# Performance work log

Measured on AMD Instinct MI355X. Metric: run time of the kernel, lower is better.

Reference implementation:

```python
import jax, jax.numpy as jnp
import numpy as np

# Faithful JAX port of approxmatch.cu / matchcost.cu (Fan et al., PointSetGeneration),
# as wrapped by emd_cuda_confidence in the torch module.

def _sqdist(xyz1, xyz2):
    # xyz1 (n,3), xyz2 (m,3) -> (n,m) squared euclidean distances
    return jnp.sum((xyz1[:, None, :] - xyz2[None, :, :]) ** 2, axis=-1)


def _approxmatch(xyz1, xyz2):
    # Iterative soft bipartite matching with annealed temperature levels
    # level = -4^j for j = 7..-1, then level = 0 (10 iterations total).
    n, m = xyz1.shape[0], xyz2.shape[0]
    sqd = _sqdist(xyz1, xyz2)  # (n, m)
    # CUDA: multiL = max(1, m/n) (int div), multiR = max(1, n/m)
    multiL = float(max(1, m // n))
    multiR = float(max(1, n // m))
    levels = jnp.asarray([-(4.0 ** j) for j in range(7, -2, -1)] + [0.0],
                         dtype=jnp.float32)
    match0 = jnp.zeros((n, m), jnp.float32)
    remL0 = jnp.full((n,), multiL, jnp.float32)
    remR0 = jnp.full((m,), multiR, jnp.float32)

    def step(carry, level):
        match, remL, remR = carry
        W = jnp.exp(level * sqd)                       # (n, m) affinity
        ratioL = remL / (1e-9 + W @ remR)              # (n,)
        ratioR = remR / (1e-9 + W.T @ ratioL)          # (m,)
        delta = W * ratioL[:, None] * ratioR[None, :]  # mass moved this level
        match = match + delta
        remL = jnp.maximum(0.0, remL - delta.sum(axis=1))
        remR = jnp.maximum(0.0, remR - delta.sum(axis=0))
        return (match, remL, remR), None

    (match, _, _), _ = jax.lax.scan(step, (match0, remL0, remR0), levels)
    return match  # (n, m)


def _matchcost(xyz1, xyz2, match):
    d = jnp.sqrt(_sqdist(xyz1, xyz2))  # euclidean distance, (n, m)
    return jnp.sum(match * d)


def setup_inputs() -> dict:
    key = jax.random.key(0)
    k1, k2 = jax.random.split(key)
    xyz1 = jax.random.normal(k1, (8, 2048, 3), dtype=jnp.float32)
    xyz2 = jax.random.normal(k2, (8, 2048, 3), dtype=jnp.float32)
    return {"xyz1": xyz1, "xyz2": xyz2}


def reference(xyz1, xyz2):
    match = jax.vmap(_approxmatch)(xyz1, xyz2)          # (b, n, m)
    cost = jax.vmap(_matchcost)(xyz1, xyz2, match)       # (b,)
    # CUDA kernel stores match with layout (b, m, n) (index k*n+l)
    return cost, jnp.swapaxes(match, 1, 2)
```

## Files before the change

### kernel.cpp

```cpp
#include <hip/hip_runtime.h>
#include <math.h>

#define B_ 8
#define N_ 2048
static constexpr int BN = B_ * N_;
static constexpr int THREADS = 256;
static constexpr int WPC = 64;
static constexpr int ROWS_PER_WG = N_ / WPC;
static constexpr int RG = 8;
static constexpr int NSTRIPE = THREADS / RG;
static constexpr int JPER = N_ / NSTRIPE;

#if __has_builtin(__builtin_amdgcn_exp2f)
#define FEXP2(x) __builtin_amdgcn_exp2f(x)
#else
#define FEXP2(x) exp2f(x)
#endif

template<int MODE>
__global__ __launch_bounds__(THREADS)
void pass_kernel(const float* __restrict__ xyz1, const float* __restrict__ xyz2,
                 float* __restrict__ ws, float* __restrict__ outCost,
                 float cA, float cB, int lvl)
{
    __shared__ float4 pts[N_];
    __shared__ float rem2[(MODE==2) ? N_ : 1];
    __shared__ float red1[4][RG][4];
    __shared__ float red2[4][RG][4];

    float* remL = ws;
    float* remR = ws + BN;
    float* ratL = ws + 2*BN;
    float* ratR = ws + 12*BN;

    const int wg = blockIdx.x;
    const int b = wg / WPC;
    const int wloc = wg - b*WPC;
    const int t = threadIdx.x;

    if (MODE==0 && wg==0 && t < B_) outCost[t] = 0.0f;

    const float* colxyz = (MODE==1) ? xyz1 : xyz2;
    const float* rowxyz = (MODE==1) ? xyz2 : xyz1;
    const float* wvec   = (MODE==1) ? (ratL + (size_t)lvl*BN)
                        : (MODE==2) ? (ratR + (size_t)lvl*BN) : nullptr;

    for (int j = t; j < N_; j += THREADS) {
        const float* p = colxyz + (size_t)(b*N_ + j)*3;
        float w = (MODE==0) ? 0.0f : wvec[b*N_ + j];
        pts[j] = make_float4(p[0], p[1], p[2], w);
        if (MODE==2) rem2[j] = remR[b*N_ + j];
    }

    const int rg = t & (RG-1);
    const int stripe = t >> 3;
    const int rowbase = wloc*ROWS_PER_WG + rg*4;
    float rx[4], ry[4], rz[4];
    #pragma unroll
    for (int r = 0; r < 4; ++r) {
        const float* q = rowxyz + (size_t)(b*N_ + rowbase + r)*3;
        rx[r] = q[0]; ry[r] = q[1]; rz[r] = q[2];
    }
    __syncthreads();

    float acc1[4] = {0.f,0.f,0.f,0.f};
    float acc2[4] = {0.f,0.f,0.f,0.f};
    const int jbase = stripe * JPER;
    const int jrot  = 2*stripe;
    for (int jj = 0; jj < JPER; ++jj) {
        const int j = jbase + ((jj + jrot) & (JPER-1));
        const float4 p = pts[j];
        float rr = 0.f;
        if (MODE==2) rr = rem2[j];
        #pragma unroll
        for (int r = 0; r < 4; ++r) {
            float dx = rx[r]-p.x, dy = ry[r]-p.y, dz = rz[r]-p.z;
            float sqd = fmaf(dx,dx, fmaf(dy,dy, dz*dz));
            float w1 = FEXP2(cA*sqd);
            if (MODE==0) acc1[r] += w1;
            else         acc1[r] = fmaf(w1, p.w, acc1[r]);
            if (MODE==2) {
                float w2 = FEXP2(cB*sqd);
                acc2[r] = fmaf(w2, rr, acc2[r]);
            }
        }
    }

    #pragma unroll
    for (int r = 0; r < 4; ++r) {
        float v = acc1[r];
        v += __shfl_xor(v, 8); v += __shfl_xor(v, 16); v += __shfl_xor(v, 32);
        acc1[r] = v;
        if (MODE==2) {
            float u = acc2[r];
            u += __shfl_xor(u, 8); u += __shfl_xor(u, 16); u += __shfl_xor(u, 32);
            acc2[r] = u;
        }
    }
    const int wave = t >> 6, lane = t & 63;
    if (lane < RG) {
        #pragma unroll
        for (int r = 0; r < 4; ++r) {
            red1[wave][lane][r] = acc1[r];
            if (MODE==2) red2[wave][lane][r] = acc2[r];
        }
    }
    __syncthreads();
    if (t < ROWS_PER_WG) {
        const int rgf = t >> 2, ri = t & 3;
        float s1 = red1[0][rgf][ri]+red1[1][rgf][ri]+red1[2][rgf][ri]+red1[3][rgf][ri];
        const int gi = b*N_ + wloc*ROWS_PER_WG + rgf*4 + ri;
        if (MODE==0) {
            ratL[gi] = 1.0f / (1e-9f + s1);
            remL[gi] = 1.0f;
            remR[gi] = 1.0f;
        } else if (MODE==1) {
            float rr  = remR[gi];
            float rat = rr / (1e-9f + s1);
            ratR[(size_t)lvl*BN + gi] = rat;
            remR[gi] = fmaxf(0.0f, rr - rat*s1);
        } else {
            float s2 = red2[0][rgf][ri]+red2[1][rgf][ri]+red2[2][rgf][ri]+red2[3][rgf][ri];
            float rl  = remL[gi];
            float rlo = ratL[(size_t)lvl*BN + gi];
            float nl  = fmaxf(0.0f, rl - rlo*s1);
            remL[gi] = nl;
            ratL[(size_t)(lvl+1)*BN + gi] = nl / (1e-9f + s2);
        }
    }
}

static constexpr int MT  = 256;
static constexpr int JCH = 256;

__global__ __launch_bounds__(MT)
void match_kernel(const float* __restrict__ xyz1, const float* __restrict__ xyz2,
                  const float* __restrict__ ws, float* __restrict__ out, float c0)
{
    __shared__ float4 pts[JCH];
    __shared__ float rr[10][JCH];
    __shared__ float cred[MT/64];

    const float* ratL = ws + 2*BN;
    const float* ratR = ws + 12*BN;
    float* outCost  = out;
    float* outMatch = out + B_;

    const int wg = blockIdx.x;
    const int b  = wg >> 6;
    const int jc = (wg >> 3) & 7;
    const int ic = wg & 7;
    const int t  = threadIdx.x;

    const int i = ic*MT + t;
    const float* q = xyz1 + (size_t)(b*N_ + i)*3;
    const float x1 = q[0], y1 = q[1], z1 = q[2];
    float RL[10];
    #pragma unroll
    for (int l = 0; l < 10; ++l) RL[l] = ratL[(size_t)l*BN + b*N_ + i];

    {
        const int gj = jc*JCH + t;
        const float* p = xyz2 + (size_t)(b*N_ + gj)*3;
        pts[t] = make_float4(p[0], p[1], p[2], 0.f);
        #pragma unroll
        for (int l = 0; l < 10; ++l) rr[l][t] = ratR[(size_t)l*BN + b*N_ + gj];
    }
    __syncthreads();

    float cost = 0.f;
    const size_t obase = (size_t)b*N_*N_ + (size_t)(jc*JCH)*N_ + (size_t)(ic*MT) + t;
    for (int jj = 0; jj < JCH; ++jj) {
        const float4 p = pts[jj];
        float dx = x1-p.x, dy = y1-p.y, dz = z1-p.z;
        float sqd = fmaf(dx,dx, fmaf(dy,dy, dz*dz));
        float m = 0.f;
        float arg = c0*sqd;
        #pragma unroll
        for (int l = 0; l < 9; ++l) {
            float w = FEXP2(arg);
            m = fmaf(w * RL[l], rr[l][jj], m);
            arg *= 0.25f;
        }
        m = fmaf(RL[9], rr[9][jj], m);
        outMatch[obase + (size_t)jj*N_] = m;
        cost = fmaf(m, sqrtf(sqd), cost);
    }

    #pragma unroll
    for (int s = 1; s < 64; s <<= 1) cost += __shfl_xor(cost, s);
    const int wave = t >> 6, lane = t & 63;
    if (lane == 0) cred[wave] = cost;
    __syncthreads();
    if (t == 0) {
        float v = cred[0]+cred[1]+cred[2]+cred[3];
        atomicAdd(outCost + b, v);
    }
}

extern "C" void kernel_launch(void* const* d_in, const int* in_sizes, int n_in,
                              void* d_out, int out_size, void* d_ws, size_t ws_size,
                              hipStream_t stream) {
    const float* xyz1 = (const float*)d_in[0];
    const float* xyz2 = (const float*)d_in[1];
    float* out = (float*)d_out;
    float* ws  = (float*)d_ws;

    const double L2E = 1.4426950408889634;
    float c[10];
    for (int l = 0; l < 9; ++l) c[l] = (float)(-pow(4.0, 7 - l) * L2E);
    c[9] = 0.0f;

    dim3 grid(B_*WPC), blk(THREADS);
    pass_kernel<0><<<grid, blk, 0, stream>>>(xyz1, xyz2, ws, out, c[0], 0.f, 0);
    for (int l = 0; l < 10; ++l) {
        pass_kernel<1><<<grid, blk, 0, stream>>>(xyz1, xyz2, ws, out, c[l], 0.f, l);
        if (l < 9)
            pass_kernel<2><<<grid, blk, 0, stream>>>(xyz1, xyz2, ws, out, c[l], c[l+1], l);
    }
    match_kernel<<<dim3(B_*64), dim3(MT), 0, stream>>>(xyz1, xyz2, ws, out, c[0]);
}
```

Baseline: 486.5 us.

## Skip underflowed exp terms, expand distances algebraically, specialize final levels, retile match

The pass kernel is rewritten so each wave handles four rows over all columns. Squared distances come from an expanded dot-product form, and wave-uniform checks skip exp evaluation when every exponent is below the float underflow threshold. The last level (c=0) is special-cased: its row sum becomes a plain sum of remR, and ratR for that level comes from a small closed-form reduction kernel instead of a full pass. The match kernel is retiled so each thread covers 4 rows over 32 columns, and it exits the level chain early once the weights underflow. It also uses nontemporal stores and derives sqrt distances from the scaled argument, which adds cancellation error from the expanded-distance form.

```diff
diff --git a/kernel.cpp b/kernel.cpp
--- a/kernel.cpp
+++ b/kernel.cpp
@@ -5,11 +5,8 @@
 #define N_ 2048
 static constexpr int BN = B_ * N_;
 static constexpr int THREADS = 256;
-static constexpr int WPC = 64;
+static constexpr int WPC = 128;
 static constexpr int ROWS_PER_WG = N_ / WPC;
-static constexpr int RG = 8;
-static constexpr int NSTRIPE = THREADS / RG;
-static constexpr int JPER = N_ / NSTRIPE;
 
 #if __has_builtin(__builtin_amdgcn_exp2f)
 #define FEXP2(x) __builtin_amdgcn_exp2f(x)
@@ -17,71 +14,79 @@
 #define FEXP2(x) exp2f(x)
 #endif
 
-template<int MODE>
-__global__ __launch_bounds__(THREADS)
+template<int MODE, bool CB0>
+__global__ __launch_bounds__(THREADS, 4)
 void pass_kernel(const float* __restrict__ xyz1, const float* __restrict__ xyz2,
                  float* __restrict__ ws, float* __restrict__ outCost,
-                 float cA, float cB, int lvl)
+                 float cA, float skipTh, int lvl)
 {
     __shared__ float4 pts[N_];
     __shared__ float rem2[(MODE==2) ? N_ : 1];
-    __shared__ float red1[4][RG][4];
-    __shared__ float red2[4][RG][4];
 
     float* remL = ws;
     float* remR = ws + BN;
     float* ratL = ws + 2*BN;
     float* ratR = ws + 12*BN;
 
-    const int wg = blockIdx.x;
-    const int b = wg / WPC;
-    const int wloc = wg - b*WPC;
-    const int t = threadIdx.x;
+    const int wg   = blockIdx.x;
+    const int b    = wg >> 7;
+    const int wloc = wg & 127;
+    const int t    = threadIdx.x;
 
     if (MODE==0 && wg==0 && t < B_) outCost[t] = 0.0f;
 
     const float* colxyz = (MODE==1) ? xyz1 : xyz2;
     const float* rowxyz = (MODE==1) ? xyz2 : xyz1;
     const float* wvec   = (MODE==1) ? (ratL + (size_t)lvl*BN)
-                        : (MODE==2) ? (ratR + (size_t)lvl*BN) : nullptr;
-
-    for (int j = t; j < N_; j += THREADS) {
+                        : (ratR + (size_t)lvl*BN);
+
+    #pragma unroll
+    for (int k = 0; k < N_/THREADS; ++k) {
+        const int j = t + k*THREADS;
         const float* p = colxyz + (size_t)(b*N_ + j)*3;
-        float w = (MODE==0) ? 0.0f : wvec[b*N_ + j];
+        float w = 0.0f;
+        if (MODE != 0) w = wvec[b*N_ + j];
         pts[j] = make_float4(p[0], p[1], p[2], w);
-        if (MODE==2) rem2[j] = remR[b*N_ + j];
-    }
-
-    const int rg = t & (RG-1);
-    const int stripe = t >> 3;
-    const int rowbase = wloc*ROWS_PER_WG + rg*4;
-    float rx[4], ry[4], rz[4];
+        if (MODE == 2) rem2[j] = remR[b*N_ + j];
+    }
+
+    const int wave = t >> 6, lane = t & 63;
+    const int rowbase = wloc*ROWS_PER_WG + wave*4;
+    float ax[4], ay[4], az[4], aq[4];
     #pragma unroll
     for (int r = 0; r < 4; ++r) {
         const float* q = rowxyz + (size_t)(b*N_ + rowbase + r)*3;
-        rx[r] = q[0]; ry[r] = q[1]; rz[r] = q[2];
+        const float qx = q[0], qy = q[1], qz = q[2];
+        ax[r] = -2.0f*cA*qx; ay[r] = -2.0f*cA*qy; az[r] = -2.0f*cA*qz;
+        aq[r] = cA * fmaf(qx,qx, fmaf(qy,qy, qz*qz));
     }
     __syncthreads();
 
     float acc1[4] = {0.f,0.f,0.f,0.f};
     float acc2[4] = {0.f,0.f,0.f,0.f};
-    const int jbase = stripe * JPER;
-    const int jrot  = 2*stripe;
-    for (int jj = 0; jj < JPER; ++jj) {
-        const int j = jbase + ((jj + jrot) & (JPER-1));
+    float sumRem = 0.f;
+
+    #pragma unroll 4
+    for (int jj = 0; jj < 32; ++jj) {
+        const int j = (lane << 5) | ((jj + lane) & 31);
         const float4 p = pts[j];
-        float rr = 0.f;
-        if (MODE==2) rr = rem2[j];
-        #pragma unroll
-        for (int r = 0; r < 4; ++r) {
-            float dx = rx[r]-p.x, dy = ry[r]-p.y, dz = rz[r]-p.z;
-            float sqd = fmaf(dx,dx, fmaf(dy,dy, dz*dz));
-            float w1 = FEXP2(cA*sqd);
-            if (MODE==0) acc1[r] += w1;
-            else         acc1[r] = fmaf(w1, p.w, acc1[r]);
-            if (MODE==2) {
-                float w2 = FEXP2(cB*sqd);
-                acc2[r] = fmaf(w2, rr, acc2[r]);
+        if (MODE==2 && CB0) sumRem += rem2[j];
+        const float cpp = cA * fmaf(p.x,p.x, fmaf(p.y,p.y, p.z*p.z));
+        float a[4];
+        #pragma unroll
+        for (int r = 0; r < 4; ++r)
+            a[r] = fmaf(ax[r],p.x, fmaf(ay[r],p.y, fmaf(az[r],p.z, cpp + aq[r])));
+        const float amax = fmaxf(fmaxf(a[0],a[1]), fmaxf(a[2],a[3]));
+        if (__any(amax >= skipTh)) {
+            float rr = 0.f;
+            if (MODE==2 && !CB0) rr = rem2[j];
+            #pragma unroll
+            for (int r = 0; r < 4; ++r) {
+                const float w1 = FEXP2(a[r]);
+                if (MODE==0) acc1[r] += w1;
+                else         acc1[r] = fmaf(w1, p.w, acc1[r]);
+                if (MODE==2 && !CB0)
+                    acc2[r] = fmaf(FEXP2(a[r]*0.25f), rr, acc2[r]);
             }
         }
     }
@@ -89,57 +94,75 @@
     #pragma unroll
     for (int r = 0; r < 4; ++r) {
         float v = acc1[r];
-        v += __shfl_xor(v, 8); v += __shfl_xor(v, 16); v += __shfl_xor(v, 32);
+        #pragma unroll
+        for (int s = 1; s < 64; s <<= 1) v += __shfl_xor(v, s);
         acc1[r] = v;
-        if (MODE==2) {
+        if (MODE==2 && !CB0) {
             float u = acc2[r];
-            u += __shfl_xor(u, 8); u += __shfl_xor(u, 16); u += __shfl_xor(u, 32);
+            #pragma unroll
+            for (int s = 1; s < 64; s <<= 1) u += __shfl_xor(u, s);
             acc2[r] = u;
         }
     }
-    const int wave = t >> 6, lane = t & 63;
-    if (lane < RG) {
+    if (MODE==2 && CB0) {
+        float u = sumRem;
+        #pragma unroll
+        for (int s = 1; s < 64; s <<= 1) u += __shfl_xor(u, s);
+        sumRem = u;
+    }
+
+    if (lane == 0) {
         #pragma unroll
         for (int r = 0; r < 4; ++r) {
-            red1[wave][lane][r] = acc1[r];
-            if (MODE==2) red2[wave][lane][r] = acc2[r];
-        }
-    }
-    __syncthreads();
-    if (t < ROWS_PER_WG) {
-        const int rgf = t >> 2, ri = t & 3;
-        float s1 = red1[0][rgf][ri]+red1[1][rgf][ri]+red1[2][rgf][ri]+red1[3][rgf][ri];
-        const int gi = b*N_ + wloc*ROWS_PER_WG + rgf*4 + ri;
-        if (MODE==0) {
-            ratL[gi] = 1.0f / (1e-9f + s1);
-            remL[gi] = 1.0f;
-            remR[gi] = 1.0f;
-        } else if (MODE==1) {
-            float rr  = remR[gi];
-            float rat = rr / (1e-9f + s1);
-            ratR[(size_t)lvl*BN + gi] = rat;
-            remR[gi] = fmaxf(0.0f, rr - rat*s1);
-        } else {
-            float s2 = red2[0][rgf][ri]+red2[1][rgf][ri]+red2[2][rgf][ri]+red2[3][rgf][ri];
-            float rl  = remL[gi];
-            float rlo = ratL[(size_t)lvl*BN + gi];
-            float nl  = fmaxf(0.0f, rl - rlo*s1);
-            remL[gi] = nl;
-            ratL[(size_t)(lvl+1)*BN + gi] = nl / (1e-9f + s2);
-        }
-    }
-}
-
-static constexpr int MT  = 256;
-static constexpr int JCH = 256;
-
-__global__ __launch_bounds__(MT)
+            const int gi = b*N_ + rowbase + r;
+            if (MODE==0) {
+                ratL[gi] = 1.0f / (1e-9f + acc1[r]);
+                remL[gi] = 1.0f;
+                remR[gi] = 1.0f;
+            } else if (MODE==1) {
+                const float rr  = remR[gi];
+                const float rat = rr / (1e-9f + acc1[r]);
+                ratR[(size_t)lvl*BN + gi] = rat;
+                remR[gi] = fmaxf(0.0f, rr - rat*acc1[r]);
+            } else {
+                const float s2  = CB0 ? sumRem : acc2[r];
+                const float rl  = remL[gi];
+                const float nl  = fmaxf(0.0f, rl - ratL[(size_t)lvl*BN + gi]*acc1[r]);
+                remL[gi] = nl;
+                ratL[(size_t)(lvl+1)*BN + gi] = nl / (1e-9f + s2);
+            }
+        }
+    }
+}
+
+__global__ __launch_bounds__(THREADS)
+void ratr9_kernel(float* __restrict__ ws)
+{
+    float* remR  = ws + BN;
+    float* ratL9 = ws + 2*BN  + (size_t)9*BN;
+    float* ratR9 = ws + 12*BN + (size_t)9*BN;
+    const int b = blockIdx.x, t = threadIdx.x;
+    __shared__ float sred[4];
+    float s = 0.f;
+    for (int k = t; k < N_; k += THREADS) s += ratL9[b*N_ + k];
+    #pragma unroll
+    for (int d = 1; d < 64; d <<= 1) s += __shfl_xor(s, d);
+    if ((t & 63) == 0) sred[t >> 6] = s;
+    __syncthreads();
+    const float inv = 1.0f / (1e-9f + (sred[0]+sred[1]+sred[2]+sred[3]));
+    for (int k = t; k < N_; k += THREADS) ratR9[b*N_ + k] = remR[b*N_ + k] * inv;
+}
+
+static constexpr int JCH = 32;
+
+__global__ __launch_bounds__(256, 4)
 void match_kernel(const float* __restrict__ xyz1, const float* __restrict__ xyz2,
-                  const float* __restrict__ ws, float* __restrict__ out, float c0)
+                  const float* __restrict__ ws, float* __restrict__ out,
+                  float c8, float invc8)
 {
     __shared__ float4 pts[JCH];
-    __shared__ float rr[10][JCH];
-    __shared__ float cred[MT/64];
+    __shared__ __align__(16) float rrs[JCH][12];
+    __shared__ float cred[4];
 
     const float* ratL = ws + 2*BN;
     const float* ratR = ws + 12*BN;
@@ -147,44 +170,70 @@
     float* outMatch = out + B_;
 
     const int wg = blockIdx.x;
-    const int b  = wg >> 6;
-    const int jc = (wg >> 3) & 7;
-    const int ic = wg & 7;
+    const int b  = wg >> 7;
+    const int ic = (wg >> 6) & 1;
+    const int jc = wg & 63;
     const int t  = threadIdx.x;
-
-    const int i = ic*MT + t;
-    const float* q = xyz1 + (size_t)(b*N_ + i)*3;
-    const float x1 = q[0], y1 = q[1], z1 = q[2];
-    float RL[10];
-    #pragma unroll
-    for (int l = 0; l < 10; ++l) RL[l] = ratL[(size_t)l*BN + b*N_ + i];
-
-    {
-        const int gj = jc*JCH + t;
-        const float* p = xyz2 + (size_t)(b*N_ + gj)*3;
+    const int jbase = jc * JCH;
+
+    if (t < JCH) {
+        const float* p = xyz2 + (size_t)(b*N_ + jbase + t)*3;
         pts[t] = make_float4(p[0], p[1], p[2], 0.f);
-        #pragma unroll
-        for (int l = 0; l < 10; ++l) rr[l][t] = ratR[(size_t)l*BN + b*N_ + gj];
+    }
+    for (int k = t; k < 10*JCH; k += 256) {
+        const int l = k >> 5, ji = k & 31;
+        rrs[ji][l] = ratR[(size_t)l*BN + b*N_ + jbase + ji];
+    }
+
+    float bx[4], by[4], bz[4], bq[4], RL[4][10];
+    #pragma unroll
+    for (int k = 0; k < 4; ++k) {
+        const int i = ic*1024 + k*256 + t;
+        const float* q = xyz1 + (size_t)(b*N_ + i)*3;
+        const float qx = q[0], qy = q[1], qz = q[2];
+        bx[k] = -2.0f*c8*qx; by[k] = -2.0f*c8*qy; bz[k] = -2.0f*c8*qz;
+        bq[k] = c8 * fmaf(qx,qx, fmaf(qy,qy, qz*qz));
+        #pragma unroll
+        for (int l = 0; l < 10; ++l) RL[k][l] = ratL[(size_t)l*BN + b*N_ + i];
     }
     __syncthreads();
 
     float cost = 0.f;
-    const size_t obase = (size_t)b*N_*N_ + (size_t)(jc*JCH)*N_ + (size_t)(ic*MT) + t;
+    const size_t ob0 = (size_t)b*N_*N_ + (size_t)jbase*N_ + (size_t)(ic*1024) + t;
+
     for (int jj = 0; jj < JCH; ++jj) {
-        const float4 p = pts[jj];
-        float dx = x1-p.x, dy = y1-p.y, dz = z1-p.z;
-        float sqd = fmaf(dx,dx, fmaf(dy,dy, dz*dz));
-        float m = 0.f;
-        float arg = c0*sqd;
-        #pragma unroll
-        for (int l = 0; l < 9; ++l) {
-            float w = FEXP2(arg);
-            m = fmaf(w * RL[l], rr[l][jj], m);
-            arg *= 0.25f;
-        }
-        m = fmaf(RL[9], rr[9][jj], m);
-        outMatch[obase + (size_t)jj*N_] = m;
-        cost = fmaf(m, sqrtf(sqd), cost);
+        const float4 p  = pts[jj];
+        const float4 rA = *(const float4*)&rrs[jj][0];
+        const float4 rB = *(const float4*)&rrs[jj][4];
+        const float4 rC = *(const float4*)&rrs[jj][8];
+        const float cpp = c8 * fmaf(p.x,p.x, fmaf(p.y,p.y, p.z*p.z));
+        float a[4], m[4], sd[4];
+        #pragma unroll
+        for (int k = 0; k < 4; ++k) {
+            a[k]  = fmaf(bx[k],p.x, fmaf(by[k],p.y, fmaf(bz[k],p.z, cpp + bq[k])));
+            sd[k] = sqrtf(a[k] * invc8);
+            m[k]  = RL[k][9] * rC.y;
+        }
+        #define DL(lv, rv) { _Pragma("unroll") \
+            for (int k = 0; k < 4; ++k) { \
+                m[k] = fmaf(FEXP2(a[k]) * RL[k][lv], rv, m[k]); a[k] *= 4.0f; } }
+        #define ALIVE __any(fmaxf(fmaxf(a[0],a[1]), fmaxf(a[2],a[3])) >= -151.0f)
+        DL(8, rC.x)
+        if (ALIVE) { DL(7, rB.w)
+         if (ALIVE) { DL(6, rB.z)
+          if (ALIVE) { DL(5, rB.y)
+           if (ALIVE) { DL(4, rB.x)
+            if (ALIVE) { DL(3, rA.w)
+             if (ALIVE) { DL(2, rA.z)
+              if (ALIVE) { DL(1, rA.y)
+               if (ALIVE) { DL(0, rA.x) } } } } } } } }
+        #undef DL
+        #undef ALIVE
+        #pragma unroll
+        for (int k = 0; k < 4; ++k) {
+            __builtin_nontemporal_store(m[k], &outMatch[ob0 + (size_t)jj*N_ + k*256]);
+            cost = fmaf(m[k], sd[k], cost);
+        }
     }
 
     #pragma unroll
@@ -192,10 +241,7 @@
     const int wave = t >> 6, lane = t & 63;
     if (lane == 0) cred[wave] = cost;
     __syncthreads();
-    if (t == 0) {
-        float v = cred[0]+cred[1]+cred[2]+cred[3];
-        atomicAdd(outCost + b, v);
-    }
+    if (t == 0) atomicAdd(outCost + b, cred[0]+cred[1]+cred[2]+cred[3]);
 }
 
 extern "C" void kernel_launch(void* const* d_in, const int* in_sizes, int n_in,
@@ -212,11 +258,14 @@
     c[9] = 0.0f;
 
     dim3 grid(B_*WPC), blk(THREADS);
-    pass_kernel<0><<<grid, blk, 0, stream>>>(xyz1, xyz2, ws, out, c[0], 0.f, 0);
-    for (int l = 0; l < 10; ++l) {
-        pass_kernel<1><<<grid, blk, 0, stream>>>(xyz1, xyz2, ws, out, c[l], 0.f, l);
-        if (l < 9)
-            pass_kernel<2><<<grid, blk, 0, stream>>>(xyz1, xyz2, ws, out, c[l], c[l+1], l);
-    }
-    match_kernel<<<dim3(B_*64), dim3(MT), 0, stream>>>(xyz1, xyz2, ws, out, c[0]);
-}
+    pass_kernel<0,false><<<grid, blk, 0, stream>>>(xyz1, xyz2, ws, out, c[0], -151.f, 0);
+    for (int l = 0; l < 9; ++l) {
+        pass_kernel<1,false><<<grid, blk, 0, stream>>>(xyz1, xyz2, ws, out, c[l], -151.f, l);
+        if (l < 8)
+            pass_kernel<2,false><<<grid, blk, 0, stream>>>(xyz1, xyz2, ws, out, c[l], -604.f, l);
+        else
+            pass_kernel<2,true><<<grid, blk, 0, stream>>>(xyz1, xyz2, ws, out, c[l], -151.f, l);
+    }
+    ratr9_kernel<<<dim3(B_), blk, 0, stream>>>(ws);
+    match_kernel<<<dim3(B_*128), dim3(256), 0, stream>>>(xyz1, xyz2, ws, out, c[8], 1.0f/c[8]);
+}
```

Result: faster. 423.4 us (-13.0%).
